# Performance work log

Hardware: AMD Instinct MI355X
Metric: run time of the kernel (lower is better)

Reference implementation:

```python
import jax, jax.numpy as jnp
import numpy as np

# --- Mamba2Simple hyperparams (from module defaults + headdim=64 hardcode) ---
D_MODEL = 512
D_STATE = 128
EXPAND = 2
HEADDIM = 64
D_INNER = EXPAND * D_MODEL          # 1024
NHEADS = D_INNER // HEADDIM         # 16
NGROUPS = 1
D_CONV = 4
CHUNK = 128                          # SSD chunk length
CONV_DIM = D_INNER + 2 * NGROUPS * D_STATE          # 1280
D_IN_PROJ = 2 * D_INNER + 2 * NGROUPS * D_STATE + NHEADS  # 2320
B_SZ, SEQ = 4, 4096
EPS = 1e-5


def setup_inputs() -> dict:
    key = jax.random.key(0)
    ks = jax.random.split(key, 8)
    x = jax.random.normal(ks[0], (B_SZ, SEQ, D_MODEL), jnp.float32)
    W_in = jax.random.normal(ks[1], (D_IN_PROJ, D_MODEL), jnp.float32) * 0.02
    conv_w = jax.random.normal(ks[2], (CONV_DIM, D_CONV), jnp.float32) * 0.1
    conv_b = jnp.zeros((CONV_DIM,), jnp.float32)
    # dt_bias = inverse-softplus of dt in [1e-3, 0.1] (mamba2 init)
    dt = jax.random.uniform(ks[3], (NHEADS,), jnp.float32, 1e-3, 0.1)
    dt_bias = jnp.log(jnp.expm1(dt))
    A_log = jnp.log(jax.random.uniform(ks[4], (NHEADS,), jnp.float32, 1.0, 16.0))
    D = jnp.ones((NHEADS,), jnp.float32)
    norm_w = jnp.ones((D_INNER,), jnp.float32)
    W_out = jax.random.normal(ks[5], (D_MODEL, D_INNER), jnp.float32) * 0.02
    return dict(x=x, W_in=W_in, conv_w=conv_w, conv_b=conv_b, dt_bias=dt_bias,
                A_log=A_log, D=D, norm_w=norm_w, W_out=W_out)


def _causal_conv(x, w, b):
    """Depthwise causal conv1d. x: (b,l,c), w: (c,K), b: (c,)."""
    lhs = x.transpose(0, 2, 1)          # (b,c,l)
    rhs = w[:, None, :]                  # (c,1,K) depthwise
    out = jax.lax.conv_general_dilated(lhs, rhs, (1,), [(D_CONV - 1, 0)],
                                       feature_group_count=CONV_DIM)
    return out.transpose(0, 2, 1) + b


def _segsum(a):
    """a: (..., T) -> (..., T, T) with out[i,j] = sum_{j<k<=i} a[k], -inf above diag."""
    T = a.shape[-1]
    cs = jnp.cumsum(a, -1)
    seg = cs[..., :, None] - cs[..., None, :]
    mask = jnp.tril(jnp.ones((T, T), bool))
    return jnp.where(mask, seg, -jnp.inf)


def _ssd(X, A, B, C):
    """Chunked SSD scan (ssd_minimal_discrete).
    X: (b,l,h,p) (= dt*x), A: (b,l,h) (= dt*A, negative), B,C: (b,l,n). ngroups=1.
    """
    b, l, h, p = X.shape
    c = l // CHUNK
    Xc = X.reshape(b, c, CHUNK, h, p)
    Ac = A.reshape(b, c, CHUNK, h).transpose(0, 3, 1, 2)   # (b,h,c,q)
    Bc = B.reshape(b, c, CHUNK, -1)                         # (b,c,q,n)
    Cc = C.reshape(b, c, CHUNK, -1)
    A_cs = jnp.cumsum(Ac, -1)                               # (b,h,c,q)
    # intra-chunk (quadratic) part
    Lmat = jnp.exp(_segsum(Ac))                             # (b,h,c,q,q) causal decay
    Y_diag = jnp.einsum('bcqn,bcsn,bhcqs,bcshp->bcqhp', Cc, Bc, Lmat, Xc)
    # per-chunk final states
    decay_states = jnp.exp(A_cs[..., -1:] - A_cs)           # (b,h,c,q)
    states = jnp.einsum('bcqn,bhcq,bcqhp->bchpn', Bc, decay_states, Xc)
    # inter-chunk recurrence (initial state = 0)
    A_last = jnp.pad(A_cs[..., -1], ((0, 0), (0, 0), (1, 0)))  # (b,h,c+1)
    decay_chunk = jnp.exp(_segsum(A_last))                     # (b,h,c+1,c+1)
    states = jnp.concatenate([jnp.zeros_like(states[:, :1]), states], axis=1)
    new_states = jnp.einsum('bhzc,bchpn->bzhpn', decay_chunk, states)
    prev_states = new_states[:, :-1]                           # (b,c,h,p,n)
    Y_off = jnp.einsum('bcqn,bchpn,bhcq->bcqhp', Cc, prev_states, jnp.exp(A_cs))
    return (Y_diag + Y_off).reshape(b, l, h, p)


def _forward(x, W_in, conv_w, conv_b, dt_bias, A_log, D, norm_w, W_out):
    bsz, L, _ = x.shape
    zxbcdt = x @ W_in.T                                   # (b,l,2320)
    z = zxbcdt[..., :D_INNER]
    xBC = zxbcdt[..., D_INNER:D_INNER + CONV_DIM]
    dt = jax.nn.softplus(zxbcdt[..., -NHEADS:] + dt_bias)  # (b,l,h)
    xBC = jax.nn.silu(_causal_conv(xBC, conv_w, conv_b))
    xs = xBC[..., :D_INNER].reshape(bsz, L, NHEADS, HEADDIM)
    Bm = xBC[..., D_INNER:D_INNER + D_STATE]               # (b,l,n)
    Cm = xBC[..., D_INNER + D_STATE:]                      # (b,l,n)
    A = -jnp.exp(A_log)                                    # (h,)
    y = _ssd(xs * dt[..., None], dt * A, Bm, Cm)           # (b,l,h,p)
    y = y + D[None, None, :, None] * xs                    # D skip
    y = y.reshape(bsz, L, D_INNER)
    # gated RMSNorm (norm_before_gate=False): rmsnorm(y * silu(z)) * w
    g = y * jax.nn.silu(z)
    g = g * jax.lax.rsqrt(jnp.mean(g * g, -1, keepdims=True) + EPS) * norm_w
    return x + g @ W_out.T                                 # residual add


def reference(x, W_in, conv_w, conv_b, dt_bias, A_log, D, norm_w, W_out):
    return _forward(x, W_in, conv_w, conv_b, dt_bias, A_log, D, norm_w, W_out)
```

## Files before the change

### kernel.cpp

```cpp
#include <hip/hip_runtime.h>
#include <hip/hip_bf16.h>

typedef __hip_bfloat16 bf16;
typedef __attribute__((ext_vector_type(8))) __bf16 bf16x8;
typedef __attribute__((ext_vector_type(4))) float f32x4;

constexpr int BSZ = 4, SEQ = 4096, DMODEL = 512;
constexpr int DSTATE = 128, HEADDIM = 64, DINNER = 1024, NHEADS = 16, CHUNK = 128;
constexpr int CONVDIM = DINNER + 2 * DSTATE;
constexpr int DINPROJ = 2 * DINNER + 2 * DSTATE + NHEADS;
constexpr int NPAD = 2432;
constexpr int MTOT = BSZ * SEQ;
constexpr int NCHUNK = SEQ / CHUNK;

constexpr size_t OFF_Z    = 0;
constexpr size_t OFF_XBC  = OFF_Z    + (size_t)MTOT * DINNER * 2;
constexpr size_t OFF_DT   = OFF_XBC  + (size_t)MTOT * CONVDIM * 2;
constexpr size_t OFF_XS   = OFF_DT   + (size_t)MTOT * NHEADS * 4;
constexpr size_t OFF_B    = OFF_XS   + (size_t)MTOT * DINNER * 2;
constexpr size_t OFF_C    = OFF_B    + (size_t)MTOT * DSTATE * 2;
constexpr size_t OFF_G    = OFF_C    + (size_t)MTOT * DSTATE * 2;
constexpr size_t OFF_ASUM = OFF_G    + (size_t)BSZ * NCHUNK * CHUNK * CHUNK * 2;
constexpr size_t WS_NEED  = OFF_ASUM + 8192;

static __device__ __forceinline__ float sigmoidf_(float x) { return 1.f / (1.f + __expf(-x)); }
static __device__ __forceinline__ unsigned short f2bf_bits(float f) {
    __hip_bfloat16 h = __float2bfloat16(f);
    return *reinterpret_cast<unsigned short*>(&h);
}
static __device__ __forceinline__ float bfbits2f(unsigned short u) {
    return __bfloat162float(*reinterpret_cast<bf16*>(&u));
}
struct us4 { unsigned short a, b, c, d; };
static __device__ __forceinline__ us4 pack4(const f32x4 v) {
    return { f2bf_bits(v[0]), f2bf_bits(v[1]), f2bf_bits(v[2]), f2bf_bits(v[3]) };
}

__global__ void k_sentinel(float* out) { out[0] = 1.0e9f; }

__global__ __launch_bounds__(256) void k_cast_x(const float* __restrict__ in, bf16* __restrict__ out, int n4) {
    int i = blockIdx.x * 256 + threadIdx.x;
    if (i >= n4) return;
    float4 f = ((const float4*)in)[i];
    us4 v = { f2bf_bits(f.x), f2bf_bits(f.y), f2bf_bits(f.z), f2bf_bits(f.w) };
    ((us4*)out)[i] = v;
}

__global__ __launch_bounds__(256) void k_cast_win(const float* __restrict__ W, bf16* __restrict__ out) {
    int i = blockIdx.x * 256 + threadIdx.x;
    if (i >= NPAD * (DMODEL / 4)) return;
    int row = i / (DMODEL / 4);
    us4 v;
    if (row < DINPROJ) {
        float4 f = ((const float4*)W)[i];
        v = { f2bf_bits(f.x), f2bf_bits(f.y), f2bf_bits(f.z), f2bf_bits(f.w) };
    } else {
        v = { 0, 0, 0, 0 };
    }
    ((us4*)out)[i] = v;
}

typedef const __attribute__((address_space(1))) void* gas_t;
typedef __attribute__((address_space(3))) void* las_t;
static __device__ __forceinline__ void gload_lds16(const void* g, void* l) {
    __builtin_amdgcn_global_load_lds((gas_t)g, (las_t)l, 16, 0, 0);
}

template<int K>
static __device__ __forceinline__ void gemm_core(
    const bf16* __restrict__ A, const bf16* __restrict__ B,
    int m0, int n0, bf16* ldsA, bf16* ldsB, f32x4 acc[4][4])
{
    const int tid = threadIdx.x;
    const int l = tid & 63, w = tid >> 6;
    const int wr = w >> 1, wc = w & 1;
    const int lq = l & 15, lk = l >> 4;
    for (int k0 = 0; k0 < K; k0 += 64) {
        #pragma unroll
        for (int i = 0; i < 4; ++i) {
            const int q = w * 32 + i * 8 + (l >> 3);
            const int ck = (l & 7) ^ (q & 7);
            gload_lds16(A + (size_t)(m0 + q) * K + k0 + ck * 8, ldsA + (w * 32 + i * 8) * 64);
            gload_lds16(B + (size_t)(n0 + q) * K + k0 + ck * 8, ldsB + (w * 32 + i * 8) * 64);
        }
        __syncthreads();
        #pragma unroll
        for (int kk = 0; kk < 64; kk += 32) {
            bf16x8 av[4], bv[4];
            #pragma unroll
            for (int f = 0; f < 4; ++f) {
                int ra = wr * 64 + f * 16 + lq;
                int pa = ((kk >> 3) + lk) ^ (ra & 7);
                av[f] = *(const bf16x8*)(ldsA + ra * 64 + pa * 8);
                int rb = wc * 64 + f * 16 + lq;
                int pb = ((kk >> 3) + lk) ^ (rb & 7);
                bv[f] = *(const bf16x8*)(ldsB + rb * 64 + pb * 8);
            }
            #pragma unroll
            for (int nf = 0; nf < 4; ++nf)
                #pragma unroll
                for (int mf = 0; mf < 4; ++mf)
                    acc[nf][mf] = __builtin_amdgcn_mfma_f32_16x16x32_bf16(bv[nf], av[mf], acc[nf][mf], 0, 0, 0);
        }
        __syncthreads();
    }
}

static __device__ __forceinline__ void swz_block(int& bx, int& by) {
    int gx = gridDim.x;
    int nwg = gx * gridDim.y;
    int wg = by * gx + bx;
    int q = nwg >> 3;
    wg = (wg & 7) * q + (wg >> 3);
    bx = wg % gx; by = wg / gx;
}

__global__ __launch_bounds__(256) void k_gemm_in(
    const bf16* __restrict__ xb, const bf16* __restrict__ Wb,
    const float* __restrict__ dt_bias,
    bf16* __restrict__ z, bf16* __restrict__ xbc, float* __restrict__ dtb)
{
    __shared__ bf16 ldsA[128 * 64];
    __shared__ bf16 ldsB[128 * 64];
    int bx = blockIdx.x, by = blockIdx.y;
    swz_block(bx, by);
    const int m0 = by * 128, n0 = bx * 128;
    f32x4 acc[4][4] = {};
    gemm_core<DMODEL>(xb, Wb, m0, n0, ldsA, ldsB, acc);
    const int l = threadIdx.x & 63, w = threadIdx.x >> 6;
    const int wr = w >> 1, wc = w & 1, lq = l & 15, lk = l >> 4;
    const int mg = m0 + wr * 64, ng = n0 + wc * 64;
    if (n0 < DINNER) {
        #pragma unroll
        for (int nf = 0; nf < 4; ++nf)
            #pragma unroll
            for (int mf = 0; mf < 4; ++mf) {
                int n = ng + nf * 16 + lk * 4;
                int m = mg + mf * 16 + lq;
                *(us4*)(z + (size_t)m * DINNER + n) = pack4(acc[nf][mf]);
            }
    } else if (n0 < DINNER + CONVDIM) {
        #pragma unroll
        for (int nf = 0; nf < 4; ++nf)
            #pragma unroll
            for (int mf = 0; mf < 4; ++mf) {
                int n = ng + nf * 16 + lk * 4 - DINNER;
                int m = mg + mf * 16 + lq;
                *(us4*)(xbc + (size_t)m * CONVDIM + n) = pack4(acc[nf][mf]);
            }
    } else {
        #pragma unroll
        for (int nf = 0; nf < 4; ++nf)
            #pragma unroll
            for (int mf = 0; mf < 4; ++mf)
                #pragma unroll
                for (int j = 0; j < 4; ++j) {
                    int n = ng + nf * 16 + lk * 4 + j;
                    int m = mg + mf * 16 + lq;
                    if (n < DINPROJ) {
                        int h = n - (DINNER + CONVDIM);
                        float t = acc[nf][mf][j] + dt_bias[h];
                        dtb[(size_t)m * NHEADS + h] = (t > 20.f) ? t : log1pf(__expf(t));
                    }
                }
    }
}

__global__ __launch_bounds__(256) void k_gemm_out(
    const bf16* __restrict__ gb, const bf16* __restrict__ Wb,
    const float* __restrict__ xres, float* __restrict__ outp)
{
    __shared__ bf16 ldsA[128 * 64];
    __shared__ bf16 ldsB[128 * 64];
    int bx = blockIdx.x, by = blockIdx.y;
    swz_block(bx, by);
    const int m0 = by * 128, n0 = bx * 128;
    f32x4 acc[4][4] = {};
    gemm_core<DINNER>(gb, Wb, m0, n0, ldsA, ldsB, acc);
    const int l = threadIdx.x & 63, w = threadIdx.x >> 6;
    const int wr = w >> 1, wc = w & 1, lq = l & 15, lk = l >> 4;
    const int mg = m0 + wr * 64, ng = n0 + wc * 64;
    #pragma unroll
    for (int nf = 0; nf < 4; ++nf)
        #pragma unroll
        for (int mf = 0; mf < 4; ++mf) {
            int n = ng + nf * 16 + lk * 4;
            int m = mg + mf * 16 + lq;
            float4 r = *(const float4*)(xres + (size_t)m * DMODEL + n);
            float4 o = { r.x + acc[nf][mf][0], r.y + acc[nf][mf][1],
                         r.z + acc[nf][mf][2], r.w + acc[nf][mf][3] };
            *(float4*)(outp + (size_t)m * DMODEL + n) = o;
        }
}

constexpr int CTOK = 8;
__global__ __launch_bounds__(320) void k_conv(
    const bf16* __restrict__ xbc, const float* __restrict__ cw, const float* __restrict__ cb,
    bf16* __restrict__ xs, bf16* __restrict__ Bm, bf16* __restrict__ Cm)
{
    const int m0 = blockIdx.x * CTOK;
    const int c4 = threadIdx.x;
    const int c = c4 * 4;
    const int l0 = m0 & 4095;
    float4 cbv = ((const float4*)cb)[c4];
    const float4 w0 = ((const float4*)cw)[c + 0];
    const float4 w1 = ((const float4*)cw)[c + 1];
    const float4 w2 = ((const float4*)cw)[c + 2];
    const float4 w3 = ((const float4*)cw)[c + 3];
    us4 rows[CTOK + 3];
    #pragma unroll
    for (int t = -3; t < CTOK; ++t) {
        int ll = l0 + t;
        if (ll >= 0) rows[t + 3] = *(const us4*)(xbc + (size_t)(m0 + t) * CONVDIM + c);
        else         rows[t + 3] = { 0, 0, 0, 0 };
    }
    #pragma unroll
    for (int t = 0; t < CTOK; ++t) {
        float a0 = cbv.x, a1 = cbv.y, a2 = cbv.z, a3 = cbv.w;
        #pragma unroll
        for (int k = 0; k < 4; ++k) {
            us4 v = rows[t + k];
            a0 += bfbits2f(v.a) * ((const float*)&w0)[k];
            a1 += bfbits2f(v.b) * ((const float*)&w1)[k];
            a2 += bfbits2f(v.c) * ((const float*)&w2)[k];
            a3 += bfbits2f(v.d) * ((const float*)&w3)[k];
        }
        us4 o = { f2bf_bits(a0 * sigmoidf_(a0)), f2bf_bits(a1 * sigmoidf_(a1)),
                  f2bf_bits(a2 * sigmoidf_(a2)), f2bf_bits(a3 * sigmoidf_(a3)) };
        int m = m0 + t;
        if (c < DINNER)               *(us4*)(xs + (size_t)m * DINNER + c) = o;
        else if (c < DINNER + DSTATE) *(us4*)(Bm + (size_t)m * DSTATE + (c - DINNER)) = o;
        else                          *(us4*)(Cm + (size_t)m * DSTATE + (c - DINNER - DSTATE)) = o;
    }
}

__global__ __launch_bounds__(64) void k_gmat(
    const bf16* __restrict__ Cm, const bf16* __restrict__ Bm, bf16* __restrict__ G)
{
    const int bc = blockIdx.z;
    const int q0 = blockIdx.x * 64, s0 = blockIdx.y * 64;
    const int row0 = bc * CHUNK;
    const int l = threadIdx.x;
    const int lq = l & 15, lk = l >> 4;
    f32x4 acc[4][4] = {};
    #pragma unroll
    for (int kc = 0; kc < 4; ++kc) {
        bf16x8 av[4], bv[4];
        #pragma unroll
        for (int f = 0; f < 4; ++f) {
            av[f] = *(const bf16x8*)(Cm + (size_t)(row0 + q0 + f * 16 + lq) * DSTATE + kc * 32 + lk * 8);
            bv[f] = *(const bf16x8*)(Bm + (size_t)(row0 + s0 + f * 16 + lq) * DSTATE + kc * 32 + lk * 8);
        }
        #pragma unroll
        for (int fr = 0; fr < 4; ++fr)
            #pragma unroll
            for (int fc = 0; fc < 4; ++fc)
                acc[fr][fc] = __builtin_amdgcn_mfma_f32_16x16x32_bf16(av[fr], bv[fc], acc[fr][fc], 0, 0, 0);
    }
    #pragma unroll
    for (int fr = 0; fr < 4; ++fr)
        #pragma unroll
        for (int fc = 0; fc < 4; ++fc)
            #pragma unroll
            for (int j = 0; j < 4; ++j) {
                int q = q0 + fr * 16 + lk * 4 + j;
                int s = s0 + fc * 16 + lq;
                G[((size_t)bc * CHUNK + q) * CHUNK + s] = __float2bfloat16(acc[fr][fc][j]);
            }
}

__global__ __launch_bounds__(256) void k_ssd(
    const bf16* __restrict__ xs , const bf16* __restrict__ Bm,
    const float* __restrict__ dtb, const float* __restrict__ A_log,
    const float* __restrict__ Dp, const bf16* __restrict__ G,
    bf16* __restrict__ y, bf16* __restrict__ states, float* __restrict__ asum)
{
    const int h = blockIdx.x, c = blockIdx.y, b = blockIdx.z;
    const int tid = threadIdx.x;
    const int l = tid & 63, w = tid >> 6;
    const int lq = l & 15, lk = l >> 4;
    __shared__ float sa[CHUNK], sdt[CHUNK], sdec[CHUNK];
    __shared__ __bf16 Xt[HEADDIM][136];
    __shared__ __bf16 Bt[DSTATE][136];
    const int row0 = b * SEQ + c * CHUNK;
    const int bc = b * NCHUNK + c;
    const float Ah = -__expf(A_log[h]);
    const float Dh = Dp[h];
    if (tid < CHUNK) {
        float d = dtb[(size_t)(row0 + tid) * NHEADS + h];
        sdt[tid] = d;
        sa[tid] = d * Ah;
    }
    __syncthreads();
    for (int off = 1; off < CHUNK; off <<= 1) {
        float v = 0.f;
        if (tid < CHUNK && tid >= off) v = sa[tid - off];
        __syncthreads();
        if (tid < CHUNK) sa[tid] += v;
        __syncthreads();
    }
    const float alast = sa[CHUNK - 1];
    if (tid < CHUNK) sdec[tid] = __expf(alast - sa[tid]);
    __syncthreads();
    {
        const int s = tid >> 1;
        const float dts = sdt[s];
        #pragma unroll
        for (int li = 0; li < 4; ++li) {
            int p0 = (tid & 1) * 8 + li * 16;
            bf16x8 v = *(const bf16x8*)(xs + (size_t)(row0 + s) * DINNER + h * HEADDIM + p0);
            #pragma unroll
            for (int i = 0; i < 8; ++i) Xt[p0 + i][s] = (__bf16)((float)v[i] * dts);
        }
        #pragma unroll
        for (int li = 0; li < 8; ++li) {
            int n0 = (tid & 1) * 8 + li * 16;
            bf16x8 v = *(const bf16x8*)(Bm + (size_t)(row0 + s) * DSTATE + n0);
            #pragma unroll
            for (int i = 0; i < 8; ++i) Bt[n0 + i][s] = v[i];
        }
    }
    __syncthreads();
    {
        const int q0 = w * 32;
        f32x4 acc[2][4] = {};
        #pragma unroll
        for (int kc = 0; kc < 4; ++kc) {
            const int sbase = kc * 32 + lk * 8;
            bf16x8 av[2];
            #pragma unroll
            for (int fr = 0; fr < 2; ++fr) {
                int q = q0 + fr * 16 + lq;
                bf16x8 g = *(const bf16x8*)(G + ((size_t)bc * CHUNK + q) * CHUNK + sbase);
                float saq = sa[q];
                bf16x8 wv;
                #pragma unroll
                for (int j = 0; j < 8; ++j) {
                    int s = sbase + j;
                    float val = (s <= q) ? __expf(saq - sa[s]) * (float)g[j] : 0.f;
                    wv[j] = (__bf16)val;
                }
                av[fr] = wv;
            }
            #pragma unroll
            for (int fc = 0; fc < 4; ++fc) {
                bf16x8 bv = *(const bf16x8*)&Xt[fc * 16 + lq][sbase];
                #pragma unroll
                for (int fr = 0; fr < 2; ++fr)
                    acc[fr][fc] = __builtin_amdgcn_mfma_f32_16x16x32_bf16(av[fr], bv, acc[fr][fc], 0, 0, 0);
            }
        }
        #pragma unroll
        for (int fr = 0; fr < 2; ++fr)
            #pragma unroll
            for (int fc = 0; fc < 4; ++fc)
                #pragma unroll
                for (int j = 0; j < 4; ++j) {
                    int q = q0 + fr * 16 + lk * 4 + j;
                    int p = fc * 16 + lq;
                    size_t idx = (size_t)(row0 + q) * DINNER + h * HEADDIM + p;
                    float xv = __bfloat162float(xs[idx]);
                    y[idx] = __float2bfloat16(acc[fr][fc][j] + Dh * xv);
                }
    }
    {
        const int n0 = w * 32;
        f32x4 acc[4][2] = {};
        #pragma unroll
        for (int kc = 0; kc < 4; ++kc) {
            const int sbase = kc * 32 + lk * 8;
            bf16x8 av[4];
            #pragma unroll
            for (int pf = 0; pf < 4; ++pf) {
                bf16x8 xv = *(const bf16x8*)&Xt[pf * 16 + lq][sbase];
                bf16x8 sc;
                #pragma unroll
                for (int j = 0; j < 8; ++j) sc[j] = (__bf16)((float)xv[j] * sdec[sbase + j]);
                av[pf] = sc;
            }
            #pragma unroll
            for (int nf = 0; nf < 2; ++nf) {
                bf16x8 bv = *(const bf16x8*)&Bt[n0 + nf * 16 + lq][sbase];
                #pragma unroll
                for (int pf = 0; pf < 4; ++pf)
                    acc[pf][nf] = __builtin_amdgcn_mfma_f32_16x16x32_bf16(av[pf], bv, acc[pf][nf], 0, 0, 0);
            }
        }
        const size_t sb = ((size_t)bc * NHEADS + h) * (HEADDIM * DSTATE);
        #pragma unroll
        for (int pf = 0; pf < 4; ++pf)
            #pragma unroll
            for (int nf = 0; nf < 2; ++nf)
                #pragma unroll
                for (int j = 0; j < 4; ++j) {
                    int p = pf * 16 + lk * 4 + j;
                    int n = n0 + nf * 16 + lq;
                    states[sb + (size_t)p * DSTATE + n] = __float2bfloat16(acc[pf][nf][j]);
                }
    }
    if (tid == 0) asum[bc * NHEADS + h] = alast;
}

__global__ __launch_bounds__(256) void k_scan(bf16* __restrict__ states, const float* __restrict__ asum)
{
    const int h = blockIdx.x, b = blockIdx.y, seg = blockIdx.z;
    const int e0 = seg * 512 + threadIdx.x;
    float P[2];
    P[0] = 0.f; P[1] = 0.f;
    for (int c = 0; c < NCHUNK; ++c) {
        size_t base = ((size_t)(b * NCHUNK + c) * NHEADS + h) * (HEADDIM * DSTATE);
        float dec = __expf(asum[(b * NCHUNK + c) * NHEADS + h]);
        #pragma unroll
        for (int j = 0; j < 2; ++j) {
            size_t e = base + e0 + j * 256;
            float sc = __bfloat162float(states[e]);
            states[e] = __float2bfloat16(P[j]);
            P[j] = dec * P[j] + sc;
        }
    }
}

__global__ __launch_bounds__(256) void k_yoff(
    const bf16* __restrict__ Cm,
    const float* __restrict__ dtb, const float* __restrict__ A_log,
    const bf16* __restrict__ states,
    bf16* __restrict__ y)
{
    const int h = blockIdx.x, c = blockIdx.y, b = blockIdx.z;
    const int tid = threadIdx.x;
    const int l = tid & 63, w = tid >> 6;
    const int lq = l & 15, lk = l >> 4;
    __shared__ float sa[CHUNK];
    const int row0 = b * SEQ + c * CHUNK;
    const int bc = b * NCHUNK + c;
    const float Ah = -__expf(A_log[h]);
    if (tid < CHUNK) {
        float d = dtb[(size_t)(row0 + tid) * NHEADS + h];
        sa[tid] = d * Ah;
    }
    __syncthreads();
    for (int off = 1; off < CHUNK; off <<= 1) {
        float v = 0.f;
        if (tid < CHUNK && tid >= off) v = sa[tid - off];
        __syncthreads();
        if (tid < CHUNK) sa[tid] += v;
        __syncthreads();
    }
    const size_t sb = ((size_t)bc * NHEADS + h) * (HEADDIM * DSTATE);
    const int q0 = w * 32;
    f32x4 acc[2][4] = {};
    #pragma unroll
    for (int kc = 0; kc < 4; ++kc) {
        const int nbase = kc * 32 + lk * 8;
        bf16x8 av[2], bv[4];
        #pragma unroll
        for (int fr = 0; fr < 2; ++fr)
            av[fr] = *(const bf16x8*)(Cm + (size_t)(row0 + q0 + fr * 16 + lq) * DSTATE + nbase);
        #pragma unroll
        for (int fc = 0; fc < 4; ++fc)
            bv[fc] = *(const bf16x8*)(states + sb + (size_t)(fc * 16 + lq) * DSTATE + nbase);
        #pragma unroll
        for (int fr = 0; fr < 2; ++fr)
            #pragma unroll
            for (int fc = 0; fc < 4; ++fc)
                acc[fr][fc] = __builtin_amdgcn_mfma_f32_16x16x32_bf16(av[fr], bv[fc], acc[fr][fc], 0, 0, 0);
    }
    #pragma unroll
    for (int fr = 0; fr < 2; ++fr)
        #pragma unroll
        for (int fc = 0; fc < 4; ++fc)
            #pragma unroll
            for (int j = 0; j < 4; ++j) {
                int q = q0 + fr * 16 + lk * 4 + j;
                int p = fc * 16 + lq;
                size_t idx = (size_t)(row0 + q) * DINNER + h * HEADDIM + p;
                float eq = __expf(sa[q]);
                y[idx] = __float2bfloat16(__bfloat162float(y[idx]) + eq * acc[fr][fc][j]);
            }
}

__global__ __launch_bounds__(256) void k_norm(
    const bf16* __restrict__ y, const bf16* __restrict__ z,
    const float* __restrict__ norm_w, bf16* __restrict__ g)
{
    const int tid = threadIdx.x;
    const int tk = tid >> 7;
    const int lane = tid & 127;
    const int m = blockIdx.x * 2 + tk;
    const int e0 = lane * 8;
    bf16x8 z8 = *(const bf16x8*)(z + (size_t)m * DINNER + e0);
    bf16x8 y8 = *(const bf16x8*)(y + (size_t)m * DINNER + e0);
    float gg[8];
    float ss = 0.f;
    #pragma unroll
    for (int i = 0; i < 8; ++i) {
        float zz = (float)z8[i];
        gg[i] = (float)y8[i] * (zz * sigmoidf_(zz));
        ss += gg[i] * gg[i];
    }
    #pragma unroll
    for (int o = 32; o > 0; o >>= 1) ss += __shfl_xor(ss, o, 64);
    __shared__ float red[4];
    if ((tid & 63) == 0) red[tid >> 6] = ss;
    __syncthreads();
    const float scale = rsqrtf((red[tk * 2] + red[tk * 2 + 1]) / DINNER + 1e-5f);
    const float4 nw0 = *(const float4*)(norm_w + e0);
    const float4 nw1 = *(const float4*)(norm_w + e0 + 4);
    bf16x8 o8;
    o8[0] = (__bf16)(gg[0] * scale * nw0.x);
    o8[1] = (__bf16)(gg[1] * scale * nw0.y);
    o8[2] = (__bf16)(gg[2] * scale * nw0.z);
    o8[3] = (__bf16)(gg[3] * scale * nw0.w);
    o8[4] = (__bf16)(gg[4] * scale * nw1.x);
    o8[5] = (__bf16)(gg[5] * scale * nw1.y);
    o8[6] = (__bf16)(gg[6] * scale * nw1.z);
    o8[7] = (__bf16)(gg[7] * scale * nw1.w);
    *(bf16x8*)(g + (size_t)m * DINNER + e0) = o8;
}

extern "C" void kernel_launch(void* const* d_in, const int* in_sizes, int n_in,
                              void* d_out, int out_size, void* d_ws, size_t ws_size,
                              hipStream_t stream) {
    const float* x       = (const float*)d_in[0];
    const float* W_in    = (const float*)d_in[1];
    const float* conv_w  = (const float*)d_in[2];
    const float* conv_b  = (const float*)d_in[3];
    const float* dt_bias = (const float*)d_in[4];
    const float* A_log   = (const float*)d_in[5];
    const float* Dp      = (const float*)d_in[6];
    const float* norm_w  = (const float*)d_in[7];
    const float* W_out   = (const float*)d_in[8];
    float* out = (float*)d_out;

    if (ws_size < WS_NEED) {
        k_sentinel<<<1, 1, 0, stream>>>(out);
        return;
    }

    char* ws = (char*)d_ws;
    bf16* z     = (bf16*)(ws + OFF_Z);
    bf16* gb    = (bf16*)(ws + OFF_Z);
    bf16* xbc   = (bf16*)(ws + OFF_XBC);
    bf16* st    = (bf16*)(ws + OFF_XBC);
    float* dtb  = (float*)(ws + OFF_DT);
    bf16* xs    = (bf16*)(ws + OFF_XS);
    bf16* yb    = (bf16*)(ws + OFF_XS);
    bf16* xb    = (bf16*)(ws + OFF_XS);
    bf16* Bm    = (bf16*)(ws + OFF_B);
    bf16* Wbin  = (bf16*)(ws + OFF_B);
    bf16* Cm    = (bf16*)(ws + OFF_C);
    bf16* G     = (bf16*)(ws + OFF_G);
    bf16* Wbout = (bf16*)(ws + OFF_G);
    float* asum = (float*)(ws + OFF_ASUM);

    k_cast_x<<<(MTOT * DMODEL / 4 + 255) / 256, 256, 0, stream>>>(x, xb, MTOT * DMODEL / 4);
    k_cast_win<<<(NPAD * DMODEL / 4 + 255) / 256, 256, 0, stream>>>(W_in, Wbin);
    k_gemm_in<<<dim3(NPAD / 128, MTOT / 128), 256, 0, stream>>>(xb, Wbin, dt_bias, z, xbc, dtb);
    k_conv<<<MTOT / CTOK, 320, 0, stream>>>(xbc, conv_w, conv_b, xs, Bm, Cm);
    k_gmat<<<dim3(2, 2, BSZ * NCHUNK), 64, 0, stream>>>(Cm, Bm, G);
    k_ssd<<<dim3(NHEADS, NCHUNK, BSZ), 256, 0, stream>>>(xs, Bm, dtb, A_log, Dp, G, yb, st, asum);
    k_cast_x<<<(DMODEL * DINNER / 4 + 255) / 256, 256, 0, stream>>>(W_out, Wbout, DMODEL * DINNER / 4);
    k_scan<<<dim3(NHEADS, BSZ, 16), 256, 0, stream>>>(st, asum);
    k_yoff<<<dim3(NHEADS, NCHUNK, BSZ), 256, 0, stream>>>(Cm, dtb, A_log, st, yb);
    k_norm<<<MTOT / 2, 256, 0, stream>>>(yb, z, norm_w, gb);
    k_gemm_out<<<dim3(DMODEL / 128, MTOT / 128), 256, 0, stream>>>(gb, Wbout, x, out);
}
```

Baseline: 269.4 us.

## Triple-buffer A tile in LDS and read B fragments directly from global

Restructures the shared GEMM core used by the in- and out-projection kernels. The A tile now goes through a three-stage LDS ring with K-step 32, with a prefetch depth of two and a single barrier per step guarded by explicit vmcnt waits. The B (weight) fragments are loaded straight from global memory into registers and no longer staged in LDS. The aim is to overlap global loads with MFMA work and halve LDS traffic and barriers, at the cost of uncoalesced, latency-exposed global B loads issued right before the MFMAs.

```diff
diff --git a/kernel.cpp b/kernel.cpp
--- a/kernel.cpp
+++ b/kernel.cpp
@@ -69,40 +69,54 @@
 template<int K>
 static __device__ __forceinline__ void gemm_core(
     const bf16* __restrict__ A, const bf16* __restrict__ B,
-    int m0, int n0, bf16* ldsA, bf16* ldsB, f32x4 acc[4][4])
-{
+    int m0, int n0, bf16* ldsA, f32x4 acc[4][4])
+{
+    constexpr int NT = K / 32;
     const int tid = threadIdx.x;
     const int l = tid & 63, w = tid >> 6;
     const int wr = w >> 1, wc = w & 1;
     const int lq = l & 15, lk = l >> 4;
-    for (int k0 = 0; k0 < K; k0 += 64) {
-        #pragma unroll
-        for (int i = 0; i < 4; ++i) {
-            const int q = w * 32 + i * 8 + (l >> 3);
-            const int ck = (l & 7) ^ (q & 7);
-            gload_lds16(A + (size_t)(m0 + q) * K + k0 + ck * 8, ldsA + (w * 32 + i * 8) * 64);
-            gload_lds16(B + (size_t)(n0 + q) * K + k0 + ck * 8, ldsB + (w * 32 + i * 8) * 64);
-        }
-        __syncthreads();
-        #pragma unroll
-        for (int kk = 0; kk < 64; kk += 32) {
-            bf16x8 av[4], bv[4];
-            #pragma unroll
-            for (int f = 0; f < 4; ++f) {
-                int ra = wr * 64 + f * 16 + lq;
-                int pa = ((kk >> 3) + lk) ^ (ra & 7);
-                av[f] = *(const bf16x8*)(ldsA + ra * 64 + pa * 8);
-                int rb = wc * 64 + f * 16 + lq;
-                int pb = ((kk >> 3) + lk) ^ (rb & 7);
-                bv[f] = *(const bf16x8*)(ldsB + rb * 64 + pb * 8);
-            }
-            #pragma unroll
-            for (int nf = 0; nf < 4; ++nf)
-                #pragma unroll
-                for (int mf = 0; mf < 4; ++mf)
-                    acc[nf][mf] = __builtin_amdgcn_mfma_f32_16x16x32_bf16(bv[nf], av[mf], acc[nf][mf], 0, 0, 0);
-        }
-        __syncthreads();
+
+    auto stage = [&](int buf, int t) {
+        const int k0 = t * 32;
+        #pragma unroll
+        for (int i = 0; i < 2; ++i) {
+            int q = w * 16 + i * 8 + (l >> 3);
+            int p = l & 7;
+            int L = p ^ (q & 7);
+            int ra = (L >> 2) * 64 + q;
+            int ck = L & 3;
+            gload_lds16(A + (size_t)(m0 + ra) * K + k0 + ck * 8,
+                        ldsA + buf * 4096 + (w * 16 + i * 8) * 64);
+        }
+    };
+
+    stage(0, 0);
+    stage(1, 1);
+    for (int t = 0; t < NT; ++t) {
+        if (t + 1 < NT) asm volatile("s_waitcnt vmcnt(2)" ::: "memory");
+        else            asm volatile("s_waitcnt vmcnt(0)" ::: "memory");
+        __builtin_amdgcn_s_barrier();
+        __builtin_amdgcn_sched_barrier(0);
+        if (t + 2 < NT) stage((t + 2) % 3, t + 2);
+        const int buf = t % 3;
+        bf16x8 av[4], bv[4];
+        #pragma unroll
+        for (int f = 0; f < 4; ++f) {
+            int rb = wc * 64 + f * 16 + lq;
+            bv[f] = *(const bf16x8*)(B + (size_t)(n0 + rb) * K + t * 32 + lk * 8);
+        }
+        #pragma unroll
+        for (int f = 0; f < 4; ++f) {
+            int ra = wr * 64 + f * 16 + lq;
+            int qa = ra & 63, La = (ra >> 6) * 4 + lk, pa = La ^ (qa & 7);
+            av[f] = *(const bf16x8*)(ldsA + buf * 4096 + qa * 64 + pa * 8);
+        }
+        #pragma unroll
+        for (int nf = 0; nf < 4; ++nf)
+            #pragma unroll
+            for (int mf = 0; mf < 4; ++mf)
+                acc[nf][mf] = __builtin_amdgcn_mfma_f32_16x16x32_bf16(bv[nf], av[mf], acc[nf][mf], 0, 0, 0);
     }
 }
 
@@ -120,13 +134,12 @@
     const float* __restrict__ dt_bias,
     bf16* __restrict__ z, bf16* __restrict__ xbc, float* __restrict__ dtb)
 {
-    __shared__ bf16 ldsA[128 * 64];
-    __shared__ bf16 ldsB[128 * 64];
+    __shared__ bf16 ldsA[3 * 4096];
     int bx = blockIdx.x, by = blockIdx.y;
     swz_block(bx, by);
     const int m0 = by * 128, n0 = bx * 128;
     f32x4 acc[4][4] = {};
-    gemm_core<DMODEL>(xb, Wb, m0, n0, ldsA, ldsB, acc);
+    gemm_core<DMODEL>(xb, Wb, m0, n0, ldsA, acc);
     const int l = threadIdx.x & 63, w = threadIdx.x >> 6;
     const int wr = w >> 1, wc = w & 1, lq = l & 15, lk = l >> 4;
     const int mg = m0 + wr * 64, ng = n0 + wc * 64;
@@ -170,13 +183,12 @@
     const bf16* __restrict__ gb, const bf16* __restrict__ Wb,
     const float* __restrict__ xres, float* __restrict__ outp)
 {
-    __shared__ bf16 ldsA[128 * 64];
-    __shared__ bf16 ldsB[128 * 64];
+    __shared__ bf16 ldsA[3 * 4096];
     int bx = blockIdx.x, by = blockIdx.y;
     swz_block(bx, by);
     const int m0 = by * 128, n0 = bx * 128;
     f32x4 acc[4][4] = {};
-    gemm_core<DINNER>(gb, Wb, m0, n0, ldsA, ldsB, acc);
+    gemm_core<DINNER>(gb, Wb, m0, n0, ldsA, acc);
     const int l = threadIdx.x & 63, w = threadIdx.x >> 6;
     const int wr = w >> 1, wc = w & 1, lq = l & 15, lk = l >> 4;
     const int mg = m0 + wr * 64, ng = n0 + wc * 64;
```

Result: slower. 325.8 us (+20.9%).
